# Kernel tuning notes

Hardware: AMD Instinct MI355X
Metric: run time of the kernel (lower is better)

The kernel has to match this reference:

```python
import jax, jax.numpy as jnp
import numpy as np

DIM = 768
NUM_HEADS = 12
HEAD_DIM = DIM // NUM_HEADS
SCALE = HEAD_DIM ** -0.5
KEEP_NUM = 160


def setup_inputs() -> dict:
    key = jax.random.key(0)
    k0, k1, k2, k3 = jax.random.split(key, 4)
    B, N, C = 64, 197, DIM
    x = jax.random.normal(k0, (B, N, C), dtype=jnp.float32)
    # torch nn.Linear weights: [out_features, in_features]
    qkv_w = jax.random.normal(k1, (3 * C, C), dtype=jnp.float32) * (C ** -0.5)
    proj_w = jax.random.normal(k2, (C, C), dtype=jnp.float32) * (C ** -0.5)
    proj_b = jax.random.normal(k3, (C,), dtype=jnp.float32) * 0.01
    return {"x": x, "qkv_w": qkv_w, "proj_w": proj_w, "proj_b": proj_b}


def reference(x, qkv_w, proj_w, proj_b):
    B, N, C = x.shape
    H, D = NUM_HEADS, HEAD_DIM
    # qkv: [B, N, 3, H, D] -> q,k,v each [B, H, N, D]
    qkv = (x @ qkv_w.T).reshape(B, N, 3, H, D)
    qkv = jnp.transpose(qkv, (2, 0, 3, 1, 4))
    q, k, v = qkv[0], qkv[1], qkv[2]
    # raw pre-softmax scores [B, H, N, N]
    attn = jnp.einsum('bhnd,bhmd->bhnm', q, k) * SCALE
    # SUM_ABS_1: CLS row of scores, abs-summed over heads -> [B, N]
    attn_weight = jnp.sum(jnp.abs(attn[:, :, 0, :]), axis=1)
    # top_pool: keep top KEEP_NUM tokens by weight, indices sorted ascending
    _, idx = jax.lax.top_k(attn_weight, KEEP_NUM)
    keep_index = jnp.sort(idx, axis=-1)
    # standard attention
    attn = jax.nn.softmax(attn, axis=-1)
    out = jnp.einsum('bhnm,bhmd->bhnd', attn, v)
    out = jnp.transpose(out, (0, 2, 1, 3)).reshape(B, N, C)
    out = out @ proj_w.T + proj_b
    return out, keep_index
```

## Files before the change

### kernel.cpp

```cpp
#include <hip/hip_runtime.h>
#include <hip/hip_bf16.h>


#define BB 64
#define NN 197
#define CC 768
#define HH 12
#define DD 64
#define KEEP 160
#define SCALE_F 0.125f
#define OUT0_ELEMS ((size_t)BB * NN * CC)
#define VST 212

typedef __attribute__((ext_vector_type(8))) short bf16x8_t;
typedef __attribute__((ext_vector_type(4))) float f32x4_t;

__device__ __forceinline__ float b2f(unsigned short u) {
  union { unsigned u; float f; } cv; cv.u = (unsigned)u << 16; return cv.f;
}
__device__ __forceinline__ unsigned short f2b(float f) {
  union { float f; unsigned u; } cv; cv.f = f;
  return (unsigned short)((cv.u + 0x7FFFu + ((cv.u >> 16) & 1u)) >> 16);
}
__device__ __forceinline__ float ldmix(const void* p, size_t i, int f32) {
  return f32 ? ((const float*)p)[i] : b2f(((const unsigned short*)p)[i]);
}
__device__ __forceinline__ bf16x8_t ld8(const unsigned short* p) {
  short4 a = *(const short4*)p;
  short4 b = *(const short4*)(p + 4);
  bf16x8_t v = {a.x, a.y, a.z, a.w, b.x, b.y, b.z, b.w};
  return v;
}
__device__ __forceinline__ void gload16(const unsigned short* g,
                                        unsigned short* s) {
  __builtin_amdgcn_global_load_lds(
      (const __attribute__((address_space(1))) void*)g,
      (__attribute__((address_space(3))) void*)s, 16, 0, 0);
}

__global__ void detect_kernel(const void* x, int* flag) {
  __shared__ int cnt;
  if (threadIdx.x == 0) cnt = 0;
  __syncthreads();
  const unsigned short* u = (const unsigned short*)x;
  int wild = 0;
  for (int i = threadIdx.x; i < 4096; i += 256) {
    int e = (u[i] >> 7) & 0xFF;
    wild += (e >= 140);
  }
  atomicAdd(&cnt, wild);
  __syncthreads();
  if (threadIdx.x == 0) *flag = (cnt > 100) ? 1 : 0;
}

__global__ void cvt_all(const void* qkv_w, const void* proj_w, const void* proj_b,
                        unsigned short* wb, unsigned short* pw, float* pbf,
                        const int* flag) {
  const int W3 = 3 * CC * CC, W1 = CC * CC;
  int i = blockIdx.x * 256 + threadIdx.x;
  const int f32 = *flag;
  if (i < W3) {
    wb[i] = f32 ? f2b(((const float*)qkv_w)[i]) : ((const unsigned short*)qkv_w)[i];
  } else if (i < W3 + W1) {
    int j = i - W3;
    pw[j] = f32 ? f2b(((const float*)proj_w)[j]) : ((const unsigned short*)proj_w)[j];
  } else if (i < W3 + W1 + CC) {
    int j = i - W3 - W1;
    pbf[j] = ldmix(proj_b, j, f32);
  }
}

__global__ void cvt_x(const void* __restrict__ x, size_t elem_off,
                      unsigned short* __restrict__ xb, int n8,
                      const int* __restrict__ flag) {
  const int i = blockIdx.x * 256 + threadIdx.x;
  if (i >= n8) return;
  const size_t src = elem_off + (size_t)i * 8;
  bf16x8_t v;
  if (*flag) {
    const float* xp = (const float*)x + src;
    float4 u0 = *(const float4*)xp;
    float4 u1 = *(const float4*)(xp + 4);
    v = bf16x8_t{(short)f2b(u0.x), (short)f2b(u0.y), (short)f2b(u0.z),
                 (short)f2b(u0.w), (short)f2b(u1.x), (short)f2b(u1.y),
                 (short)f2b(u1.z), (short)f2b(u1.w)};
  } else {
    v = *(const bf16x8_t*)((const unsigned short*)x + src);
  }
  *(bf16x8_t*)(xb + (size_t)i * 8) = v;
}

__global__ __launch_bounds__(256, 4) void qkv_gemm(
    const unsigned short* __restrict__ xb,
    const unsigned short* __restrict__ wb,
    unsigned short* __restrict__ qkvc, int Mc, int bc, int nRow) {
  const int xcd = blockIdx.x & 7;
  const int seq = blockIdx.x >> 3;
  const int colt = seq % 18;
  const int rowt = (seq / 18) * 8 + xcd;
  if (rowt >= nRow) return;
  const int m0 = rowt * 128;
  const int n0 = colt * 128;

  __shared__ unsigned short As[8192];
  __shared__ unsigned short Bs[8192];
  const int lane = threadIdx.x & 63;
  const int wave = threadIdx.x >> 6;
  const int l16  = lane & 15;
  const int quad = lane >> 4;
  const int wm = wave >> 1, wn = wave & 1;

  const int rS   = wave * 16 + (lane >> 2);
  const int koff = (lane & 3) * 8;
  int grA0 = m0 + rS;       if (grA0 >= Mc) grA0 = Mc - 1;
  int grA1 = m0 + rS + 64;  if (grA1 >= Mc) grA1 = Mc - 1;
  const unsigned short* gA0 = xb + (size_t)grA0 * CC + koff;
  const unsigned short* gA1 = xb + (size_t)grA1 * CC + koff;
  const unsigned short* gB0 = wb + (size_t)(n0 + rS) * CC + koff;
  const unsigned short* gB1 = wb + (size_t)(n0 + rS + 64) * CC + koff;
  unsigned short* const sA0 = As + wave * 512;
  unsigned short* const sA1 = As + 2048 + wave * 512;
  unsigned short* const sB0 = Bs + wave * 512;
  unsigned short* const sB1 = Bs + 2048 + wave * 512;

  gload16(gA0, sA0); gload16(gA1, sA1);
  gload16(gB0, sB0); gload16(gB1, sB1);
  gA0 += 32; gA1 += 32; gB0 += 32; gB1 += 32;

  f32x4_t acc[4][4] = {};
  #pragma unroll 2
  for (int kt = 0; kt < 24; kt++) {
    const int ro = (kt & 1) << 12;
    const int so = ro ^ 4096;
    if (kt < 23) {
      gload16(gA0, sA0 + so); gload16(gA1, sA1 + so);
      gload16(gB0, sB0 + so); gload16(gB1, sB1 + so);
      gA0 += 32; gA1 += 32; gB0 += 32; gB1 += 32;
      asm volatile("s_waitcnt vmcnt(4)" ::: "memory");
    } else {
      asm volatile("s_waitcnt vmcnt(0)" ::: "memory");
    }
    __builtin_amdgcn_s_barrier();
    bf16x8_t afr[4], bfr[4];
    #pragma unroll
    for (int r = 0; r < 4; r++)
      afr[r] = *(const bf16x8_t*)&As[ro + (wm * 4 + r) * 512 + l16 * 32 + quad * 8];
    #pragma unroll
    for (int c = 0; c < 4; c++)
      bfr[c] = *(const bf16x8_t*)&Bs[ro + (wn * 4 + c) * 512 + l16 * 32 + quad * 8];
    asm volatile("s_waitcnt lgkmcnt(0)" ::: "memory");
    __builtin_amdgcn_s_barrier();
    #pragma unroll
    for (int r = 0; r < 4; r++)
      #pragma unroll
      for (int c = 0; c < 4; c++)
        acc[r][c] = __builtin_amdgcn_mfma_f32_16x16x32_bf16(afr[r], bfr[c],
                                                            acc[r][c], 0, 0, 0);
  }
  #pragma unroll
  for (int c = 0; c < 4; c++) {
    const int col = n0 + wn * 64 + c * 16 + l16;
    const int s = col / CC;
    const int rem = col - s * CC;
    const int hc = rem >> 6, d = rem & 63;
    #pragma unroll
    for (int r = 0; r < 4; r++) {
      #pragma unroll
      for (int i = 0; i < 4; i++) {
        const int m = m0 + wm * 64 + r * 16 + quad * 4 + i;
        if (m < Mc) {
          const int bb = m / NN, n = m - bb * NN;
          qkvc[((((size_t)s * bc + bb) * HH + hc) * NN + n) * DD + d] =
              f2b(acc[r][c][i]);
        }
      }
    }
  }
}

__global__ __launch_bounds__(256, 4) void proj_gemm(
    const unsigned short* __restrict__ Yc,
    const unsigned short* __restrict__ pw,
    const float* __restrict__ pbf,
    void* __restrict__ out, size_t out_off, int Mc, int nRow,
    const int* __restrict__ flag) {
  const int xcd = blockIdx.x & 7;
  const int seq = blockIdx.x >> 3;
  const int colt = seq % 6;
  const int rowt = (seq / 6) * 8 + xcd;
  if (rowt >= nRow) return;
  const int m0 = rowt * 128;
  const int n0 = colt * 128;

  __shared__ unsigned short As[8192];
  __shared__ unsigned short Bs[8192];
  const int lane = threadIdx.x & 63;
  const int wave = threadIdx.x >> 6;
  const int l16  = lane & 15;
  const int quad = lane >> 4;
  const int wm = wave >> 1, wn = wave & 1;

  const int rS   = wave * 16 + (lane >> 2);
  const int koff = (lane & 3) * 8;
  int grA0 = m0 + rS;       if (grA0 >= Mc) grA0 = Mc - 1;
  int grA1 = m0 + rS + 64;  if (grA1 >= Mc) grA1 = Mc - 1;
  const unsigned short* gA0 = Yc + (size_t)grA0 * CC + koff;
  const unsigned short* gA1 = Yc + (size_t)grA1 * CC + koff;
  const unsigned short* gB0 = pw + (size_t)(n0 + rS) * CC + koff;
  const unsigned short* gB1 = pw + (size_t)(n0 + rS + 64) * CC + koff;
  unsigned short* const sA0 = As + wave * 512;
  unsigned short* const sA1 = As + 2048 + wave * 512;
  unsigned short* const sB0 = Bs + wave * 512;
  unsigned short* const sB1 = Bs + 2048 + wave * 512;

  gload16(gA0, sA0); gload16(gA1, sA1);
  gload16(gB0, sB0); gload16(gB1, sB1);
  gA0 += 32; gA1 += 32; gB0 += 32; gB1 += 32;

  f32x4_t acc[4][4] = {};
  #pragma unroll 2
  for (int kt = 0; kt < 24; kt++) {
    const int ro = (kt & 1) << 12;
    const int so = ro ^ 4096;
    if (kt < 23) {
      gload16(gA0, sA0 + so); gload16(gA1, sA1 + so);
      gload16(gB0, sB0 + so); gload16(gB1, sB1 + so);
      gA0 += 32; gA1 += 32; gB0 += 32; gB1 += 32;
      asm volatile("s_waitcnt vmcnt(4)" ::: "memory");
    } else {
      asm volatile("s_waitcnt vmcnt(0)" ::: "memory");
    }
    __builtin_amdgcn_s_barrier();
    bf16x8_t afr[4], bfr[4];
    #pragma unroll
    for (int r = 0; r < 4; r++)
      afr[r] = *(const bf16x8_t*)&As[ro + (wm * 4 + r) * 512 + l16 * 32 + quad * 8];
    #pragma unroll
    for (int c = 0; c < 4; c++)
      bfr[c] = *(const bf16x8_t*)&Bs[ro + (wn * 4 + c) * 512 + l16 * 32 + quad * 8];
    asm volatile("s_waitcnt lgkmcnt(0)" ::: "memory");
    __builtin_amdgcn_s_barrier();
    #pragma unroll
    for (int r = 0; r < 4; r++)
      #pragma unroll
      for (int c = 0; c < 4; c++)
        acc[r][c] = __builtin_amdgcn_mfma_f32_16x16x32_bf16(afr[r], bfr[c],
                                                            acc[r][c], 0, 0, 0);
  }
  const int f32 = *flag;
  #pragma unroll
  for (int c = 0; c < 4; c++) {
    const int col = n0 + wn * 64 + c * 16 + l16;
    const float bv = pbf[col];
    #pragma unroll
    for (int r = 0; r < 4; r++) {
      #pragma unroll
      for (int i = 0; i < 4; i++) {
        const int m = m0 + wm * 64 + r * 16 + quad * 4 + i;
        if (m < Mc) {
          const float val = acc[r][c][i] + bv;
          const size_t oi = out_off + (size_t)m * CC + col;
          if (f32) ((float*)out)[oi] = val;
          else ((unsigned short*)out)[oi] = f2b(val);
        }
      }
    }
  }
}

__global__ __launch_bounds__(256, 3) void attn_kernel(
    const unsigned short* __restrict__ qkvc, int bc,
    unsigned short* __restrict__ Yc) {
  const int bh = blockIdx.x;
  const int bb = bh / HH;
  const int h  = bh % HH;
  const size_t mat = (size_t)bc * HH * NN * DD;
  const unsigned short* q = qkvc + ((size_t)bb * HH + h) * NN * DD;
  const unsigned short* k = q + mat;
  const unsigned short* v = q + 2 * mat;

  __shared__ unsigned short Vt[DD * VST];
  __shared__ unsigned short Pl[4][16 * VST];

  const int lane = threadIdx.x & 63;
  const int wave = threadIdx.x >> 6;
  const int l16  = lane & 15;
  const int quad = lane >> 4;

  #pragma unroll
  for (int it = 0; it < 53; it++) {
    const int key = it * 4 + wave;
    unsigned short val = (key < NN) ? v[(size_t)key * DD + lane]
                                    : (unsigned short)0;
    Vt[lane * VST + key] = val;
  }
  __syncthreads();

  unsigned short* Pw = &Pl[wave][0];

  for (int it = 0; it < 4; it++) {
    const int si = it * 4 + wave;
    if (si >= 13) break;
    const int q0 = si * 16;

    int qrow = q0 + l16; if (qrow >= NN) qrow = NN - 1;
    const unsigned short* qp = q + (size_t)qrow * DD + quad * 8;
    const bf16x8_t aq0 = *(const bf16x8_t*)qp;
    const bf16x8_t aq1 = *(const bf16x8_t*)(qp + 32);

    f32x4_t sc[13];
    #pragma unroll
    for (int ct = 0; ct < 13; ct++) {
      int key = ct * 16 + l16; if (key >= NN) key = NN - 1;
      const unsigned short* kp = k + (size_t)key * DD + quad * 8;
      const bf16x8_t b0 = *(const bf16x8_t*)kp;
      const bf16x8_t b1 = *(const bf16x8_t*)(kp + 32);
      f32x4_t t = {0.f, 0.f, 0.f, 0.f};
      t = __builtin_amdgcn_mfma_f32_16x16x32_bf16(aq0, b0, t, 0, 0, 0);
      t = __builtin_amdgcn_mfma_f32_16x16x32_bf16(aq1, b1, t, 0, 0, 0);
      sc[ct] = t;
    }

    float inv_l[4];
    #pragma unroll
    for (int i = 0; i < 4; i++) {
      float m = -1e30f;
      #pragma unroll
      for (int ct = 0; ct < 13; ct++)
        if (ct < 12 || l16 < 5) m = fmaxf(m, sc[ct][i] * SCALE_F);
      #pragma unroll
      for (int d = 1; d < 16; d <<= 1) m = fmaxf(m, __shfl_xor(m, d, 64));
      float s = 0.f;
      #pragma unroll
      for (int ct = 0; ct < 13; ct++) {
        const float p = (ct < 12 || l16 < 5) ? __expf(sc[ct][i] * SCALE_F - m)
                                             : 0.f;
        sc[ct][i] = p;
        s += p;
      }
      #pragma unroll
      for (int d = 1; d < 16; d <<= 1) s += __shfl_xor(s, d, 64);
      inv_l[i] = 1.0f / s;
    }

    #pragma unroll
    for (int i = 0; i < 4; i++) {
      const int ro = (quad * 4 + i) * VST;
      #pragma unroll
      for (int ct = 0; ct < 13; ct++)
        Pw[ro + ct * 16 + l16] = f2b(sc[ct][i]);
    }

    f32x4_t oc[4] = {};
    #pragma unroll
    for (int ks = 0; ks < 6; ks++) {
      const bf16x8_t ap = ld8(&Pw[l16 * VST + ks * 32 + quad * 8]);
      #pragma unroll
      for (int dt = 0; dt < 4; dt++) {
        const bf16x8_t bv = ld8(&Vt[(dt * 16 + l16) * VST + ks * 32 + quad * 8]);
        oc[dt] = __builtin_amdgcn_mfma_f32_16x16x32_bf16(ap, bv, oc[dt], 0, 0, 0);
      }
    }
    {
      const bf16x8_t zz = {};
      bf16x8_t ap = zz;
      if (quad < 2) ap = ld8(&Pw[l16 * VST + 192 + quad * 8]);
      #pragma unroll
      for (int dt = 0; dt < 4; dt++) {
        bf16x8_t bv = zz;
        if (quad < 2) bv = ld8(&Vt[(dt * 16 + l16) * VST + 192 + quad * 8]);
        oc[dt] = __builtin_amdgcn_mfma_f32_16x16x32_bf16(ap, bv, oc[dt], 0, 0, 0);
      }
    }

    #pragma unroll
    for (int i = 0; i < 4; i++) {
      const int n = q0 + quad * 4 + i;
      if (n < NN) {
        unsigned short* yp = Yc + ((size_t)bb * NN + n) * CC + h * DD;
        #pragma unroll
        for (int dt = 0; dt < 4; dt++)
          yp[dt * 16 + l16] = f2b(oc[dt][i] * inv_l[i]);
      }
    }
  }
}

__global__ __launch_bounds__(256, 4) void qcls_kernel(
    const void* __restrict__ x, const void* __restrict__ qkv_w,
    float* __restrict__ qc, const int* __restrict__ flag) {
  const int idx = blockIdx.x * 4 + (threadIdx.x >> 6);
  if (idx >= BB * CC) return;
  const int b = idx / CC, i = idx - b * CC;
  const int lane = threadIdx.x & 63;
  const int f32 = *flag;
  const size_t xr = (size_t)b * NN * CC;
  const size_t wr = (size_t)i * CC;
  float p = 0.f;
  #pragma unroll
  for (int j = 0; j < 12; j++)
    p += ldmix(x, xr + j * 64 + lane, f32) * ldmix(qkv_w, wr + j * 64 + lane, f32);
  #pragma unroll
  for (int m = 32; m; m >>= 1) p += __shfl_xor(p, m, 64);
  if (lane == 0) qc[(size_t)b * CC + i] = p;
}

__global__ __launch_bounds__(256, 2) void gmat_kernel(
    const void* __restrict__ qkv_w, const float* __restrict__ qc,
    float* __restrict__ g, const int* __restrict__ flag) {
  const int h = blockIdx.x, c0 = blockIdx.y * 128;
  const int f32 = *flag;
  __shared__ float Wt[64][128];
  __shared__ float qh[64][64];
  for (int t = threadIdx.x; t < 64 * 128; t += 256) {
    const int d = t >> 7, c = t & 127;
    Wt[d][c] = ldmix(qkv_w, (size_t)(CC + h * DD + d) * CC + c0 + c, f32);
  }
  for (int t = threadIdx.x; t < 64 * 64; t += 256) {
    const int b = t >> 6, d = t & 63;
    qh[b][d] = qc[(size_t)b * CC + h * DD + d];
  }
  __syncthreads();
  const int c = threadIdx.x & 127;
  const int bg = (threadIdx.x >> 7) * 32;
  for (int bi = 0; bi < 32; bi++) {
    const int b = bg + bi;
    float a = 0.f;
    #pragma unroll
    for (int d = 0; d < 64; d++) a += qh[b][d] * Wt[d][c];
    g[((size_t)b * HH + h) * CC + c0 + c] = a;
  }
}

__global__ __launch_bounds__(256, 4) void score_kernel(
    const void* __restrict__ x, const float* __restrict__ g,
    float* __restrict__ wscore, const int* __restrict__ flag) {
  const int idx = blockIdx.x * 4 + (threadIdx.x >> 6);
  if (idx >= BB * NN) return;
  const int b = idx / NN, n = idx - b * NN;
  const int lane = threadIdx.x & 63;
  const int f32 = *flag;
  const size_t xr = ((size_t)b * NN + n) * CC;
  float xv[12];
  #pragma unroll
  for (int j = 0; j < 12; j++) xv[j] = ldmix(x, xr + j * 64 + lane, f32);
  const float* gb = g + (size_t)b * HH * CC;
  float acc = 0.f;
  #pragma unroll
  for (int h = 0; h < HH; h++) {
    const float* gh = gb + (size_t)h * CC;
    float p = 0.f;
    #pragma unroll
    for (int j = 0; j < 12; j++) p += xv[j] * gh[j * 64 + lane];
    #pragma unroll
    for (int m = 32; m; m >>= 1) p += __shfl_xor(p, m, 64);
    acc += fabsf(p);
  }
  if (lane == 0) wscore[(size_t)b * NN + n] = acc;
}

__global__ __launch_bounds__(256, 4) void rank_kernel(
    const float* __restrict__ wscore, void* __restrict__ out,
    const int* __restrict__ flag) {
  const int b = blockIdx.x;
  const int f32 = *flag;
  __shared__ float wgt[NN];
  __shared__ int   rank[NN];
  if (threadIdx.x < NN) wgt[threadIdx.x] = wscore[(size_t)b * NN + threadIdx.x];
  __syncthreads();
  const int n = threadIdx.x;
  if (n < NN) {
    float wi = wgt[n];
    int rk = 0;
    for (int j = 0; j < NN; j++) {
      float wj = wgt[j];
      rk += (wj > wi) || (wj == wi && j < n);
    }
    rank[n] = rk;
  }
  __syncthreads();
  if (n < NN && rank[n] < KEEP) {
    int pos = 0;
    for (int j = 0; j < n; j++) pos += (rank[j] < KEEP);
    const size_t oi = OUT0_ELEMS + (size_t)b * KEEP + pos;
    if (f32) ((float*)out)[oi] = (float)n;
    else ((unsigned short*)out)[oi] = f2b((float)n);
  }
}

extern "C" void kernel_launch(void* const* d_in, const int* in_sizes, int n_in,
                              void* d_out, int out_size, void* d_ws, size_t ws_size,
                              hipStream_t stream) {
  const void* x      = d_in[0];
  const void* qkv_w  = d_in[1];
  const void* proj_w = d_in[2];
  const void* proj_b = d_in[3];

  char* wsb = (char*)d_ws;
  int* flag = (int*)wsb;
  unsigned short* wb  = (unsigned short*)(wsb + 256);
  unsigned short* pw  = (unsigned short*)(wsb + 256 + 3538944);
  float* pbf    = (float*)(wsb + 256 + 3538944 + 1179648);
  float* qc     = (float*)(wsb + 256 + 3538944 + 1179648 + 4096);
  float* g      = qc + (size_t)BB * CC;
  float* wscore = g + (size_t)BB * HH * CC;
  const size_t fixed = 256 + 3538944 + 1179648 + 4096 + 196608 + 2359296 + 51200;
  char* chunk = wsb + fixed;

  const size_t per_batch = (size_t)NN * CC * 2
                         + 3ull * HH * NN * DD * 2
                         + (size_t)NN * CC * 2;
  int Bc = BB;
  while (Bc > 1 && fixed + (size_t)Bc * per_batch > ws_size) Bc >>= 1;

  unsigned short* xb   = (unsigned short*)chunk;
  unsigned short* qkvc = xb + (size_t)Bc * NN * CC;
  unsigned short* Yc   = qkvc + 3ull * Bc * HH * NN * DD;

  detect_kernel<<<1, 256, 0, stream>>>(x, flag);
  const int cvt_n = 3 * CC * CC + CC * CC + CC;
  cvt_all<<<(cvt_n + 255) / 256, 256, 0, stream>>>(qkv_w, proj_w, proj_b,
                                                   wb, pw, pbf, flag);

  qcls_kernel<<<(BB * CC + 3) / 4, 256, 0, stream>>>(x, qkv_w, qc, flag);
  gmat_kernel<<<dim3(HH, 6), 256, 0, stream>>>(qkv_w, qc, g, flag);
  score_kernel<<<(BB * NN + 3) / 4, 256, 0, stream>>>(x, g, wscore, flag);
  rank_kernel<<<BB, 256, 0, stream>>>(wscore, d_out, flag);

  const int nChunks = (BB + Bc - 1) / Bc;
  for (int cb = 0; cb < nChunks; cb++) {
    const int b0 = cb * Bc;
    const int bc = (BB - b0 < Bc) ? (BB - b0) : Bc;
    const int Mc = bc * NN;
    const int n8 = Mc * CC / 8;
    cvt_x<<<(n8 + 255) / 256, 256, 0, stream>>>(
        x, (size_t)b0 * NN * CC, xb, n8, flag);
    const int nRowQ = (Mc + 127) / 128;
    const int gridQ = 8 * 18 * ((nRowQ + 7) / 8);
    qkv_gemm<<<gridQ, 256, 0, stream>>>(xb, wb, qkvc, Mc, bc, nRowQ);
    attn_kernel<<<dim3(bc * HH), 256, 0, stream>>>(qkvc, bc, Yc);
    const int gridP = 8 * 6 * ((nRowQ + 7) / 8);
    proj_gemm<<<gridP, 256, 0, stream>>>(
        Yc, pw, pbf, d_out, (size_t)b0 * NN * CC, Mc, nRowQ, flag);
  }
}
```

Baseline: 382.0 us.

## Switch QKV and projection GEMMs to 256x256 tiles with 8-wave pipelined core

Measured after the change: 389.2 us. Within noise of the previous version (+1.9%).

```diff
diff --git a/kernel.cpp b/kernel.cpp
--- a/kernel.cpp
+++ b/kernel.cpp
@@ -36,6 +36,106 @@
   __builtin_amdgcn_global_load_lds(
       (const __attribute__((address_space(1))) void*)g,
       (__attribute__((address_space(3))) void*)s, 16, 0, 0);
+}
+
+#define MM(A,B,C) __builtin_amdgcn_mfma_f32_16x16x32_bf16(A,B,C,0,0,0)
+
+#define MFMA16(AB) \
+  asm volatile("s_barrier" ::: "memory"); \
+  asm volatile("s_waitcnt lgkmcnt(0)" ::: "memory"); \
+  __builtin_amdgcn_s_setprio(1); \
+  acc[AB+0][0] = MM(a0,b0,acc[AB+0][0]); acc[AB+0][1] = MM(a0,b1,acc[AB+0][1]); \
+  acc[AB+0][2] = MM(a0,b2,acc[AB+0][2]); acc[AB+0][3] = MM(a0,b3,acc[AB+0][3]); \
+  acc[AB+1][0] = MM(a1,b0,acc[AB+1][0]); acc[AB+1][1] = MM(a1,b1,acc[AB+1][1]); \
+  acc[AB+1][2] = MM(a1,b2,acc[AB+1][2]); acc[AB+1][3] = MM(a1,b3,acc[AB+1][3]); \
+  acc[AB+2][0] = MM(a2,b0,acc[AB+2][0]); acc[AB+2][1] = MM(a2,b1,acc[AB+2][1]); \
+  acc[AB+2][2] = MM(a2,b2,acc[AB+2][2]); acc[AB+2][3] = MM(a2,b3,acc[AB+2][3]); \
+  acc[AB+3][0] = MM(a3,b0,acc[AB+3][0]); acc[AB+3][1] = MM(a3,b1,acc[AB+3][1]); \
+  acc[AB+3][2] = MM(a3,b2,acc[AB+3][2]); acc[AB+3][3] = MM(a3,b3,acc[AB+3][3]); \
+  __builtin_amdgcn_s_setprio(0); \
+  asm volatile("s_barrier" ::: "memory");
+
+#define LDSLD(off) (*(const bf16x8_t*)&lds[(off)])
+
+__device__ __forceinline__ void gemm256_core(
+    const unsigned short* __restrict__ Ab, const unsigned short* __restrict__ Bb,
+    int m0, int n0, int Mc, unsigned short* lds, f32x4_t (&acc)[8][4]) {
+  const int tid  = threadIdx.x;
+  const int lane = tid & 63;
+  const int w    = tid >> 6;
+  const int l16  = lane & 15;
+  const int quad = lane >> 4;
+  const int wm   = w >> 2, wn = w & 3;
+
+  const int rsub = w * 16 + (lane >> 2);
+  const int ksub = (lane & 3) * 8;
+  int rA0 = m0 + rsub;       if (rA0 >= Mc) rA0 = Mc - 1;
+  int rA1 = m0 + 128 + rsub; if (rA1 >= Mc) rA1 = Mc - 1;
+  const unsigned short* pA0 = Ab + (size_t)rA0 * CC + ksub;
+  const unsigned short* pA1 = Ab + (size_t)rA1 * CC + ksub;
+  const unsigned short* pB0 = Bb + (size_t)(n0 + rsub) * CC + ksub;
+  const unsigned short* pB1 = Bb + (size_t)(n0 + 128 + rsub) * CC + ksub;
+
+  const int wof  = w * 512;
+  const int aoff = wm * 4096 + l16 * 32 + quad * 8;
+  const int boff = 16384 + wn * 2048 + l16 * 32 + quad * 8;
+
+  gload16(pA0 +  0, lds +     0 + wof); gload16(pA1 +  0, lds +  4096 + wof);
+  gload16(pB0 +  0, lds + 16384 + wof); gload16(pB1 +  0, lds + 20480 + wof);
+  gload16(pA0 + 32, lds +  8192 + wof); gload16(pA1 + 32, lds + 12288 + wof);
+  gload16(pB0 + 32, lds + 24576 + wof); gload16(pB1 + 32, lds + 28672 + wof);
+  gload16(pA0 + 64, lds + 32768 + wof); gload16(pA1 + 64, lds + 36864 + wof);
+  gload16(pB0 + 64, lds + 49152 + wof); gload16(pB1 + 64, lds + 53248 + wof);
+  asm volatile("s_waitcnt vmcnt(4)" ::: "memory");
+  asm volatile("s_barrier" ::: "memory");
+
+  #pragma unroll 2
+  for (int kt = 0; kt < 12; kt++) {
+    const int dof  = (kt & 1) << 15;
+    const int sof  = dof ^ 32768;
+    const int ko01 = kt * 64 + 96;
+    const int ko23 = kt * 64 + 128;
+    bf16x8_t a0, a1, a2, a3, b0, b1, b2, b3;
+
+    b0 = LDSLD(dof + boff);        b1 = LDSLD(dof + boff + 512);
+    b2 = LDSLD(dof + boff + 1024); b3 = LDSLD(dof + boff + 1536);
+    a0 = LDSLD(dof + aoff);        a1 = LDSLD(dof + aoff + 512);
+    a2 = LDSLD(dof + aoff + 1024); a3 = LDSLD(dof + aoff + 1536);
+    if (kt < 11) {
+      gload16(pA0 + ko01, lds + sof +  8192 + wof);
+      gload16(pA1 + ko01, lds + sof + 12288 + wof);
+    }
+    MFMA16(0)
+
+    a0 = LDSLD(dof + aoff + 2048); a1 = LDSLD(dof + aoff + 2560);
+    a2 = LDSLD(dof + aoff + 3072); a3 = LDSLD(dof + aoff + 3584);
+    if (kt < 11) {
+      gload16(pB0 + ko01, lds + sof + 24576 + wof);
+      gload16(pB1 + ko01, lds + sof + 28672 + wof);
+    }
+    MFMA16(4)
+
+    b0 = LDSLD(dof + 8192 + boff);        b1 = LDSLD(dof + 8192 + boff + 512);
+    b2 = LDSLD(dof + 8192 + boff + 1024); b3 = LDSLD(dof + 8192 + boff + 1536);
+    a0 = LDSLD(dof + 8192 + aoff);        a1 = LDSLD(dof + 8192 + aoff + 512);
+    a2 = LDSLD(dof + 8192 + aoff + 1024); a3 = LDSLD(dof + 8192 + aoff + 1536);
+    if (kt < 10) {
+      gload16(pA0 + ko23, lds + dof +    0 + wof);
+      gload16(pA1 + ko23, lds + dof + 4096 + wof);
+    }
+    MFMA16(0)
+
+    a0 = LDSLD(dof + 8192 + aoff + 2048); a1 = LDSLD(dof + 8192 + aoff + 2560);
+    a2 = LDSLD(dof + 8192 + aoff + 3072); a3 = LDSLD(dof + 8192 + aoff + 3584);
+    if (kt < 10) {
+      gload16(pB0 + ko23, lds + dof + 16384 + wof);
+      gload16(pB1 + ko23, lds + dof + 20480 + wof);
+      asm volatile("s_waitcnt vmcnt(4)" ::: "memory");
+    } else {
+      asm volatile("s_waitcnt vmcnt(0)" ::: "memory");
+    }
+    MFMA16(4)
+  }
 }
 
 __global__ void detect_kernel(const void* x, int* flag) {
@@ -90,73 +190,27 @@
   *(bf16x8_t*)(xb + (size_t)i * 8) = v;
 }
 
-__global__ __launch_bounds__(256, 4) void qkv_gemm(
+__global__ __launch_bounds__(512, 1) void qkv_gemm(
     const unsigned short* __restrict__ xb,
     const unsigned short* __restrict__ wb,
     unsigned short* __restrict__ qkvc, int Mc, int bc, int nRow) {
   const int xcd = blockIdx.x & 7;
   const int seq = blockIdx.x >> 3;
-  const int colt = seq % 18;
-  const int rowt = (seq / 18) * 8 + xcd;
+  const int colt = seq % 9;
+  const int rowt = (seq / 9) * 8 + xcd;
   if (rowt >= nRow) return;
-  const int m0 = rowt * 128;
-  const int n0 = colt * 128;
-
-  __shared__ unsigned short As[8192];
-  __shared__ unsigned short Bs[8192];
+  const int m0 = rowt * 256;
+  const int n0 = colt * 256;
+
+  __shared__ unsigned short lds[65536];
+  f32x4_t acc[8][4] = {};
+  gemm256_core(xb, wb, m0, n0, Mc, lds, acc);
+
   const int lane = threadIdx.x & 63;
-  const int wave = threadIdx.x >> 6;
+  const int w    = threadIdx.x >> 6;
   const int l16  = lane & 15;
   const int quad = lane >> 4;
-  const int wm = wave >> 1, wn = wave & 1;
-
-  const int rS   = wave * 16 + (lane >> 2);
-  const int koff = (lane & 3) * 8;
-  int grA0 = m0 + rS;       if (grA0 >= Mc) grA0 = Mc - 1;
-  int grA1 = m0 + rS + 64;  if (grA1 >= Mc) grA1 = Mc - 1;
-  const unsigned short* gA0 = xb + (size_t)grA0 * CC + koff;
-  const unsigned short* gA1 = xb + (size_t)grA1 * CC + koff;
-  const unsigned short* gB0 = wb + (size_t)(n0 + rS) * CC + koff;
-  const unsigned short* gB1 = wb + (size_t)(n0 + rS + 64) * CC + koff;
-  unsigned short* const sA0 = As + wave * 512;
-  unsigned short* const sA1 = As + 2048 + wave * 512;
-  unsigned short* const sB0 = Bs + wave * 512;
-  unsigned short* const sB1 = Bs + 2048 + wave * 512;
-
-  gload16(gA0, sA0); gload16(gA1, sA1);
-  gload16(gB0, sB0); gload16(gB1, sB1);
-  gA0 += 32; gA1 += 32; gB0 += 32; gB1 += 32;
-
-  f32x4_t acc[4][4] = {};
-  #pragma unroll 2
-  for (int kt = 0; kt < 24; kt++) {
-    const int ro = (kt & 1) << 12;
-    const int so = ro ^ 4096;
-    if (kt < 23) {
-      gload16(gA0, sA0 + so); gload16(gA1, sA1 + so);
-      gload16(gB0, sB0 + so); gload16(gB1, sB1 + so);
-      gA0 += 32; gA1 += 32; gB0 += 32; gB1 += 32;
-      asm volatile("s_waitcnt vmcnt(4)" ::: "memory");
-    } else {
-      asm volatile("s_waitcnt vmcnt(0)" ::: "memory");
-    }
-    __builtin_amdgcn_s_barrier();
-    bf16x8_t afr[4], bfr[4];
-    #pragma unroll
-    for (int r = 0; r < 4; r++)
-      afr[r] = *(const bf16x8_t*)&As[ro + (wm * 4 + r) * 512 + l16 * 32 + quad * 8];
-    #pragma unroll
-    for (int c = 0; c < 4; c++)
-      bfr[c] = *(const bf16x8_t*)&Bs[ro + (wn * 4 + c) * 512 + l16 * 32 + quad * 8];
-    asm volatile("s_waitcnt lgkmcnt(0)" ::: "memory");
-    __builtin_amdgcn_s_barrier();
-    #pragma unroll
-    for (int r = 0; r < 4; r++)
-      #pragma unroll
-      for (int c = 0; c < 4; c++)
-        acc[r][c] = __builtin_amdgcn_mfma_f32_16x16x32_bf16(afr[r], bfr[c],
-                                                            acc[r][c], 0, 0, 0);
-  }
+  const int wm   = w >> 2, wn = w & 3;
   #pragma unroll
   for (int c = 0; c < 4; c++) {
     const int col = n0 + wn * 64 + c * 16 + l16;
@@ -164,21 +218,22 @@
     const int rem = col - s * CC;
     const int hc = rem >> 6, d = rem & 63;
     #pragma unroll
-    for (int r = 0; r < 4; r++) {
+    for (int rr = 0; rr < 8; rr++) {
+      const int mb = m0 + wm * 128 + (rr >> 2) * 64 + (rr & 3) * 16 + quad * 4;
       #pragma unroll
       for (int i = 0; i < 4; i++) {
-        const int m = m0 + wm * 64 + r * 16 + quad * 4 + i;
+        const int m = mb + i;
         if (m < Mc) {
           const int bb = m / NN, n = m - bb * NN;
           qkvc[((((size_t)s * bc + bb) * HH + hc) * NN + n) * DD + d] =
-              f2b(acc[r][c][i]);
+              f2b(acc[rr][c][i]);
         }
       }
     }
   }
 }
 
-__global__ __launch_bounds__(256, 4) void proj_gemm(
+__global__ __launch_bounds__(512, 1) void proj_gemm(
     const unsigned short* __restrict__ Yc,
     const unsigned short* __restrict__ pw,
     const float* __restrict__ pbf,
@@ -186,79 +241,34 @@
     const int* __restrict__ flag) {
   const int xcd = blockIdx.x & 7;
   const int seq = blockIdx.x >> 3;
-  const int colt = seq % 6;
-  const int rowt = (seq / 6) * 8 + xcd;
+  const int colt = seq % 3;
+  const int rowt = (seq / 3) * 8 + xcd;
   if (rowt >= nRow) return;
-  const int m0 = rowt * 128;
-  const int n0 = colt * 128;
-
-  __shared__ unsigned short As[8192];
-  __shared__ unsigned short Bs[8192];
+  const int m0 = rowt * 256;
+  const int n0 = colt * 256;
+
+  __shared__ unsigned short lds[65536];
+  f32x4_t acc[8][4] = {};
+  gemm256_core(Yc, pw, m0, n0, Mc, lds, acc);
+
   const int lane = threadIdx.x & 63;
-  const int wave = threadIdx.x >> 6;
+  const int w    = threadIdx.x >> 6;
   const int l16  = lane & 15;
   const int quad = lane >> 4;
-  const int wm = wave >> 1, wn = wave & 1;
-
-  const int rS   = wave * 16 + (lane >> 2);
-  const int koff = (lane & 3) * 8;
-  int grA0 = m0 + rS;       if (grA0 >= Mc) grA0 = Mc - 1;
-  int grA1 = m0 + rS + 64;  if (grA1 >= Mc) grA1 = Mc - 1;
-  const unsigned short* gA0 = Yc + (size_t)grA0 * CC + koff;
-  const unsigned short* gA1 = Yc + (size_t)grA1 * CC + koff;
-  const unsigned short* gB0 = pw + (size_t)(n0 + rS) * CC + koff;
-  const unsigned short* gB1 = pw + (size_t)(n0 + rS + 64) * CC + koff;
-  unsigned short* const sA0 = As + wave * 512;
-  unsigned short* const sA1 = As + 2048 + wave * 512;
-  unsigned short* const sB0 = Bs + wave * 512;
-  unsigned short* const sB1 = Bs + 2048 + wave * 512;
-
-  gload16(gA0, sA0); gload16(gA1, sA1);
-  gload16(gB0, sB0); gload16(gB1, sB1);
-  gA0 += 32; gA1 += 32; gB0 += 32; gB1 += 32;
-
-  f32x4_t acc[4][4] = {};
-  #pragma unroll 2
-  for (int kt = 0; kt < 24; kt++) {
-    const int ro = (kt & 1) << 12;
-    const int so = ro ^ 4096;
-    if (kt < 23) {
-      gload16(gA0, sA0 + so); gload16(gA1, sA1 + so);
-      gload16(gB0, sB0 + so); gload16(gB1, sB1 + so);
-      gA0 += 32; gA1 += 32; gB0 += 32; gB1 += 32;
-      asm volatile("s_waitcnt vmcnt(4)" ::: "memory");
-    } else {
-      asm volatile("s_waitcnt vmcnt(0)" ::: "memory");
-    }
-    __builtin_amdgcn_s_barrier();
-    bf16x8_t afr[4], bfr[4];
-    #pragma unroll
-    for (int r = 0; r < 4; r++)
-      afr[r] = *(const bf16x8_t*)&As[ro + (wm * 4 + r) * 512 + l16 * 32 + quad * 8];
-    #pragma unroll
-    for (int c = 0; c < 4; c++)
-      bfr[c] = *(const bf16x8_t*)&Bs[ro + (wn * 4 + c) * 512 + l16 * 32 + quad * 8];
-    asm volatile("s_waitcnt lgkmcnt(0)" ::: "memory");
-    __builtin_amdgcn_s_barrier();
-    #pragma unroll
-    for (int r = 0; r < 4; r++)
-      #pragma unroll
-      for (int c = 0; c < 4; c++)
-        acc[r][c] = __builtin_amdgcn_mfma_f32_16x16x32_bf16(afr[r], bfr[c],
-                                                            acc[r][c], 0, 0, 0);
-  }
+  const int wm   = w >> 2, wn = w & 3;
   const int f32 = *flag;
   #pragma unroll
   for (int c = 0; c < 4; c++) {
     const int col = n0 + wn * 64 + c * 16 + l16;
     const float bv = pbf[col];
     #pragma unroll
-    for (int r = 0; r < 4; r++) {
+    for (int rr = 0; rr < 8; rr++) {
+      const int mb = m0 + wm * 128 + (rr >> 2) * 64 + (rr & 3) * 16 + quad * 4;
       #pragma unroll
       for (int i = 0; i < 4; i++) {
-        const int m = m0 + wm * 64 + r * 16 + quad * 4 + i;
+        const int m = mb + i;
         if (m < Mc) {
-          const float val = acc[r][c][i] + bv;
+          const float val = acc[rr][c][i] + bv;
           const size_t oi = out_off + (size_t)m * CC + col;
           if (f32) ((float*)out)[oi] = val;
           else ((unsigned short*)out)[oi] = f2b(val);
@@ -535,12 +545,12 @@
     const int n8 = Mc * CC / 8;
     cvt_x<<<(n8 + 255) / 256, 256, 0, stream>>>(
         x, (size_t)b0 * NN * CC, xb, n8, flag);
-    const int nRowQ = (Mc + 127) / 128;
-    const int gridQ = 8 * 18 * ((nRowQ + 7) / 8);
-    qkv_gemm<<<gridQ, 256, 0, stream>>>(xb, wb, qkvc, Mc, bc, nRowQ);
+    const int nRowQ = (Mc + 255) / 256;
+    const int gridQ = 8 * 9 * ((nRowQ + 7) / 8);
+    qkv_gemm<<<gridQ, 512, 0, stream>>>(xb, wb, qkvc, Mc, bc, nRowQ);
     attn_kernel<<<dim3(bc * HH), 256, 0, stream>>>(qkvc, bc, Yc);
-    const int gridP = 8 * 6 * ((nRowQ + 7) / 8);
-    proj_gemm<<<gridP, 256, 0, stream>>>(
+    const int gridP = 8 * 3 * ((nRowQ + 7) / 8);
+    proj_gemm<<<gridP, 512, 0, stream>>>(
         Yc, pw, pbf, d_out, (size_t)b0 * NN * CC, Mc, nRowQ, flag);
   }
 }
```
